# Performance work log

Hardware: AMD Instinct MI355X
Metric: run time of the kernel (lower is better)

Reference implementation:

```python
import jax, jax.numpy as jnp
import numpy as np

B, IN_DIM, OUT_DIM = 4096, 8192, 8192

# Each of the 16 gates op_i(a,b) is affine in (1, a, b, a*b).
# Rows: [const, coef_a, coef_b, coef_ab] for gate i = 0..15.
GATE_COEF = np.array([
    [0.,  0.,  0.,  0.],   # 0: zeros
    [0.,  0.,  0.,  1.],   # 1: a*b
    [0.,  1.,  0., -1.],   # 2: a - a*b
    [0.,  1.,  0.,  0.],   # 3: a
    [0.,  0.,  1., -1.],   # 4: b - a*b
    [0.,  0.,  1.,  0.],   # 5: b
    [0.,  1.,  1., -2.],   # 6: a + b - 2ab (xor)
    [0.,  1.,  1., -1.],   # 7: a + b - ab (or)
    [1., -1., -1.,  1.],   # 8: 1 - (a + b - ab)
    [1., -1., -1.,  2.],   # 9: 1 - (a + b - 2ab)
    [1.,  0., -1.,  0.],   # 10: 1 - b
    [1.,  0., -1.,  1.],   # 11: 1 - b + ab
    [1., -1.,  0.,  0.],   # 12: 1 - a
    [1., -1.,  0.,  1.],   # 13: 1 - a + ab
    [1.,  0.,  0., -1.],   # 14: 1 - ab
    [1.,  0.,  0.,  0.],   # 15: ones
], dtype=np.float32)


def setup_inputs() -> dict:
    key = jax.random.key(0)
    k1, k2, k3, k4 = jax.random.split(key, 4)
    x = jax.random.uniform(k1, (B, IN_DIM), dtype=jnp.float32)
    weights = jax.random.normal(k2, (OUT_DIM, 16), dtype=jnp.float32)
    idx0 = jax.random.randint(k3, (OUT_DIM,), 0, IN_DIM)
    idx1 = jax.random.randint(k4, (OUT_DIM,), 0, IN_DIM)
    return {"x": x, "weights": weights, "idx0": idx0, "idx1": idx1}


def reference(x, weights, idx0, idx1):
    # training path: soft mixture over 16 gates
    p = jax.nn.softmax(weights, axis=-1)          # [out_dim, 16]
    c = p @ jnp.asarray(GATE_COEF)                # [out_dim, 4]: sum_i p_i * op_i collapsed
    a = x[:, idx0]                                # [B, out_dim]
    b = x[:, idx1]                                # [B, out_dim]
    return c[:, 0] + c[:, 1] * a + c[:, 2] * b + c[:, 3] * (a * b)
```

## Files before the change

kernel.cpp:

```cpp
#include <hip/hip_runtime.h>

#define IN_DIM 8192
#define OUT_DIM 8192
#define NROWS 4096
#define THREADS 512
#define GRID 512
#define RPB (NROWS / GRID)
#define JG (OUT_DIM / (THREADS * 4))
#define SV (IN_DIM / (THREADS * 4))

static_assert(GRID * RPB == NROWS, "row partition");
static_assert(JG * THREADS * 4 == OUT_DIM, "col partition");
static_assert(SV * THREADS * 4 == IN_DIM, "stage partition");

typedef float v4f __attribute__((ext_vector_type(4)));

#define BLOCK_SYNC_LDS()                                   \
  do {                                                     \
    asm volatile("s_waitcnt lgkmcnt(0)" ::: "memory");     \
    __builtin_amdgcn_s_barrier();                          \
    asm volatile("" ::: "memory");                         \
  } while (0)

__device__ __constant__ float GATE_COEF[16][4] = {
    {0.f, 0.f, 0.f, 0.f}, {0.f, 0.f, 0.f, 1.f}, {0.f, 1.f, 0.f, -1.f}, {0.f, 1.f, 0.f, 0.f},
    {0.f, 0.f, 1.f, -1.f}, {0.f, 0.f, 1.f, 0.f}, {0.f, 1.f, 1.f, -2.f}, {0.f, 1.f, 1.f, -1.f},
    {1.f, -1.f, -1.f, 1.f}, {1.f, -1.f, -1.f, 2.f}, {1.f, 0.f, -1.f, 0.f}, {1.f, 0.f, -1.f, 1.f},
    {1.f, -1.f, 0.f, 0.f}, {1.f, -1.f, 0.f, 1.f}, {1.f, 0.f, 0.f, -1.f}, {1.f, 0.f, 0.f, 0.f}};

__global__ __launch_bounds__(256) void compute_c_kernel(const float* __restrict__ w,
                                                        float* __restrict__ cp) {
  int j = blockIdx.x * blockDim.x + threadIdx.x;
  if (j >= OUT_DIM) return;
  const float4* wv = (const float4*)(w + (size_t)j * 16);
  float4 w0 = wv[0], w1 = wv[1], w2 = wv[2], w3 = wv[3];
  float wa[16] = {w0.x, w0.y, w0.z, w0.w, w1.x, w1.y, w1.z, w1.w,
                  w2.x, w2.y, w2.z, w2.w, w3.x, w3.y, w3.z, w3.w};
  float m = wa[0];
#pragma unroll
  for (int k = 1; k < 16; ++k) m = fmaxf(m, wa[k]);
  float p[16];
  float s = 0.f;
#pragma unroll
  for (int k = 0; k < 16; ++k) {
    p[k] = __expf(wa[k] - m);
    s += p[k];
  }
  float inv = 1.f / s;
  float c0 = 0.f, c1 = 0.f, c2 = 0.f, c3 = 0.f;
#pragma unroll
  for (int k = 0; k < 16; ++k) {
    c0 = fmaf(p[k], GATE_COEF[k][0], c0);
    c1 = fmaf(p[k], GATE_COEF[k][1], c1);
    c2 = fmaf(p[k], GATE_COEF[k][2], c2);
    c3 = fmaf(p[k], GATE_COEF[k][3], c3);
  }
  cp[j] = c0 * inv;
  cp[j + OUT_DIM] = c1 * inv;
  cp[j + 2 * OUT_DIM] = c2 * inv;
  cp[j + 3 * OUT_DIM] = c3 * inv;
}

__global__ __launch_bounds__(THREADS, 4) void gate_persist(
    const float* __restrict__ x, const float* __restrict__ cp,
    const int* __restrict__ idx0, const int* __restrict__ idx1,
    float* __restrict__ out) {
  __shared__ __align__(16) float buf[2][IN_DIM];
  const int tid = threadIdx.x;
  const int r0 = blockIdx.x * RPB;

  int4 i0[JG], i1[JG];
#pragma unroll
  for (int g = 0; g < JG; ++g) {
    const int j = tid * 4 + g * (THREADS * 4);
    i0[g] = *(const int4*)(idx0 + j);
    i1[g] = *(const int4*)(idx1 + j);
  }

  const float* c0p = cp;
  const float* c1p = cp + OUT_DIM;
  const float* c2p = cp + 2 * OUT_DIM;
  const float* c3p = cp + 3 * OUT_DIM;

  v4f ra[SV];
  const float* x0 = x + (size_t)r0 * IN_DIM;
#pragma unroll
  for (int t = 0; t < SV; ++t)
    ra[t] = __builtin_nontemporal_load((const v4f*)x0 + tid + t * THREADS);
#pragma unroll
  for (int t = 0; t < SV; ++t) ((v4f*)buf[0])[tid + t * THREADS] = ra[t];
#pragma unroll
  for (int t = 0; t < SV; ++t)
    ra[t] = __builtin_nontemporal_load((const v4f*)(x0 + IN_DIM) + tid + t * THREADS);
  BLOCK_SYNC_LDS();

#pragma unroll 1
  for (int p = 0; p < RPB; ++p) {
    if (p + 1 < RPB) {
      v4f* dst = (v4f*)buf[(p + 1) & 1];
#pragma unroll
      for (int t = 0; t < SV; ++t) dst[tid + t * THREADS] = ra[t];
    }
    if (p + 2 < RPB) {
      const float* xs = x + (size_t)(r0 + p + 2) * IN_DIM;
#pragma unroll
      for (int t = 0; t < SV; ++t)
        ra[t] = __builtin_nontemporal_load((const v4f*)xs + tid + t * THREADS);
    }
    const float* bufc = buf[p & 1];
    float* o = out + (size_t)(r0 + p) * OUT_DIM;
#pragma unroll
    for (int g = 0; g < JG; ++g) {
      const int j = tid * 4 + g * (THREADS * 4);
      const v4f c0v = *(const v4f*)(c0p + j);
      const v4f c1v = *(const v4f*)(c1p + j);
      const v4f c2v = *(const v4f*)(c2p + j);
      const v4f c3v = *(const v4f*)(c3p + j);
      const int4 ia = i0[g], ib = i1[g];
      v4f a, b;
      a.x = bufc[ia.x]; a.y = bufc[ia.y]; a.z = bufc[ia.z]; a.w = bufc[ia.w];
      b.x = bufc[ib.x]; b.y = bufc[ib.y]; b.z = bufc[ib.z]; b.w = bufc[ib.w];
      const v4f r = c0v + c1v * a + c2v * b + c3v * (a * b);
      __builtin_nontemporal_store(r, (v4f*)(o + j));
    }
    BLOCK_SYNC_LDS();
  }
}

extern "C" void kernel_launch(void* const* d_in, const int* in_sizes, int n_in,
                              void* d_out, int out_size, void* d_ws, size_t ws_size,
                              hipStream_t stream) {
  const float* x = (const float*)d_in[0];
  const float* weights = (const float*)d_in[1];
  const int* idx0 = (const int*)d_in[2];
  const int* idx1 = (const int*)d_in[3];
  float* out = (float*)d_out;
  float* cp = (float*)d_ws;

  compute_c_kernel<<<OUT_DIM / 256, 256, 0, stream>>>(weights, cp);
  gate_persist<<<GRID, THREADS, 0, stream>>>(x, cp, idx0, idx1, out);
}
```

Measured before the change: 238.0 us.

## Process x rows in pairs to reuse coefficients and indices per LDS pass

```diff
diff --git a/kernel.cpp b/kernel.cpp
--- a/kernel.cpp
+++ b/kernel.cpp
@@ -6,6 +6,7 @@
 #define THREADS 512
 #define GRID 512
 #define RPB (NROWS / GRID)
+#define NP (RPB / 2)
 #define JG (OUT_DIM / (THREADS * 4))
 #define SV (IN_DIM / (THREADS * 4))
 
@@ -61,11 +62,11 @@
   cp[j + 3 * OUT_DIM] = c3 * inv;
 }
 
-__global__ __launch_bounds__(THREADS, 4) void gate_persist(
+__global__ __launch_bounds__(THREADS, 4) void gate_pairs(
     const float* __restrict__ x, const float* __restrict__ cp,
     const int* __restrict__ idx0, const int* __restrict__ idx1,
     float* __restrict__ out) {
-  __shared__ __align__(16) float buf[2][IN_DIM];
+  __shared__ __align__(16) float buf[2 * IN_DIM];
   const int tid = threadIdx.x;
   const int r0 = blockIdx.x * RPB;
 
@@ -82,33 +83,33 @@
   const float* c2p = cp + 2 * OUT_DIM;
   const float* c3p = cp + 3 * OUT_DIM;
 
-  v4f ra[SV];
-  const float* x0 = x + (size_t)r0 * IN_DIM;
+  v4f ra[2 * SV];
+  {
+    const float* xr = x + (size_t)r0 * IN_DIM;
 #pragma unroll
-  for (int t = 0; t < SV; ++t)
-    ra[t] = __builtin_nontemporal_load((const v4f*)x0 + tid + t * THREADS);
+    for (int row = 0; row < 2; ++row)
 #pragma unroll
-  for (int t = 0; t < SV; ++t) ((v4f*)buf[0])[tid + t * THREADS] = ra[t];
+      for (int t = 0; t < SV; ++t)
+        ra[row * SV + t] =
+            __builtin_nontemporal_load((const v4f*)(xr + row * IN_DIM) + tid + t * THREADS);
 #pragma unroll
-  for (int t = 0; t < SV; ++t)
-    ra[t] = __builtin_nontemporal_load((const v4f*)(x0 + IN_DIM) + tid + t * THREADS);
+    for (int row = 0; row < 2; ++row)
+#pragma unroll
+      for (int t = 0; t < SV; ++t)
+        ((v4f*)(buf + row * IN_DIM))[tid + t * THREADS] = ra[row * SV + t];
+    const float* xn = x + (size_t)(r0 + 2) * IN_DIM;
+#pragma unroll
+    for (int row = 0; row < 2; ++row)
+#pragma unroll
+      for (int t = 0; t < SV; ++t)
+        ra[row * SV + t] =
+            __builtin_nontemporal_load((const v4f*)(xn + row * IN_DIM) + tid + t * THREADS);
+  }
   BLOCK_SYNC_LDS();
 
 #pragma unroll 1
-  for (int p = 0; p < RPB; ++p) {
-    if (p + 1 < RPB) {
-      v4f* dst = (v4f*)buf[(p + 1) & 1];
-#pragma unroll
-      for (int t = 0; t < SV; ++t) dst[tid + t * THREADS] = ra[t];
-    }
-    if (p + 2 < RPB) {
-      const float* xs = x + (size_t)(r0 + p + 2) * IN_DIM;
-#pragma unroll
-      for (int t = 0; t < SV; ++t)
-        ra[t] = __builtin_nontemporal_load((const v4f*)xs + tid + t * THREADS);
-    }
-    const float* bufc = buf[p & 1];
-    float* o = out + (size_t)(r0 + p) * OUT_DIM;
+  for (int p = 0; p < NP; ++p) {
+    float* o0 = out + (size_t)(r0 + 2 * p) * OUT_DIM;
 #pragma unroll
     for (int g = 0; g < JG; ++g) {
       const int j = tid * 4 + g * (THREADS * 4);
@@ -117,11 +118,34 @@
       const v4f c2v = *(const v4f*)(c2p + j);
       const v4f c3v = *(const v4f*)(c3p + j);
       const int4 ia = i0[g], ib = i1[g];
-      v4f a, b;
-      a.x = bufc[ia.x]; a.y = bufc[ia.y]; a.z = bufc[ia.z]; a.w = bufc[ia.w];
-      b.x = bufc[ib.x]; b.y = bufc[ib.y]; b.z = bufc[ib.z]; b.w = bufc[ib.w];
-      const v4f r = c0v + c1v * a + c2v * b + c3v * (a * b);
-      __builtin_nontemporal_store(r, (v4f*)(o + j));
+      v4f a0, b0, a1, b1;
+      a0.x = buf[ia.x]; a0.y = buf[ia.y]; a0.z = buf[ia.z]; a0.w = buf[ia.w];
+      b0.x = buf[ib.x]; b0.y = buf[ib.y]; b0.z = buf[ib.z]; b0.w = buf[ib.w];
+      a1.x = buf[IN_DIM + ia.x]; a1.y = buf[IN_DIM + ia.y];
+      a1.z = buf[IN_DIM + ia.z]; a1.w = buf[IN_DIM + ia.w];
+      b1.x = buf[IN_DIM + ib.x]; b1.y = buf[IN_DIM + ib.y];
+      b1.z = buf[IN_DIM + ib.z]; b1.w = buf[IN_DIM + ib.w];
+      const v4f r0v = c0v + c1v * a0 + c2v * b0 + c3v * (a0 * b0);
+      const v4f r1v = c0v + c1v * a1 + c2v * b1 + c3v * (a1 * b1);
+      __builtin_nontemporal_store(r0v, (v4f*)(o0 + j));
+      __builtin_nontemporal_store(r1v, (v4f*)(o0 + OUT_DIM + j));
+    }
+    BLOCK_SYNC_LDS();
+    if (p + 1 < NP) {
+#pragma unroll
+      for (int row = 0; row < 2; ++row)
+#pragma unroll
+        for (int t = 0; t < SV; ++t)
+          ((v4f*)(buf + row * IN_DIM))[tid + t * THREADS] = ra[row * SV + t];
+    }
+    if (p + 2 < NP) {
+      const float* xn = x + (size_t)(r0 + 2 * (p + 2)) * IN_DIM;
+#pragma unroll
+      for (int row = 0; row < 2; ++row)
+#pragma unroll
+        for (int t = 0; t < SV; ++t)
+          ra[row * SV + t] =
+              __builtin_nontemporal_load((const v4f*)(xn + row * IN_DIM) + tid + t * THREADS);
     }
     BLOCK_SYNC_LDS();
   }
@@ -138,5 +162,5 @@
   float* cp = (float*)d_ws;
 
   compute_c_kernel<<<OUT_DIM / 256, 256, 0, stream>>>(weights, cp);
-  gate_persist<<<GRID, THREADS, 0, stream>>>(x, cp, idx0, idx1, out);
+  gate_pairs<<<GRID, THREADS, 0, stream>>>(x, cp, idx0, idx1, out);
 }
```

After: 266.3 us. 1.12x slower.
